# Kernel tuning notes

Measured on AMD Instinct MI355X. Metric: run time of the kernel, lower is better.

Reference implementation:

```python
import jax, jax.numpy as jnp
import numpy as np

B, L, K, I, O = 4, 10000, 16, 256, 256


def setup_inputs() -> dict:
    key = jax.random.key(0)
    k1, k2, k3 = jax.random.split(key, 3)
    x = jax.random.normal(k1, (B, L, I), dtype=jnp.float32)
    index_tensor = jax.random.randint(k2, (L, K), 0, L, dtype=jnp.int64)
    stdv = 0.5
    mask = jax.random.uniform(k3, (K, I, O), dtype=jnp.float32, minval=-stdv, maxval=stdv)
    bias = jnp.zeros((O,), dtype=jnp.float32)
    return {"x": x, "index_tensor": index_tensor, "mask": mask, "bias": bias}


def reference(x, index_tensor, mask, bias):
    # torch: expand x to [b,l,l,i], gather along dim2 with index[l,k] -> [b,l,k,i]
    # equivalent: per output node n, neighbors x[:, index_tensor[n, j], :]
    gathered = x[:, index_tensor, :]            # [b, l, k, i]
    # flatten(k,i) @ flatten(mask: [k*i, o]) == einsum over k,i
    y = jnp.einsum('blki,kio->blo', gathered, mask) + bias
    return y
```

## Files before the change

### kernel.cpp

```cpp
#include <hip/hip_runtime.h>

#define Bdim 4
#define Ldim 10000
#define Kdim 16
#define Idim 256
#define Odim 256

typedef __attribute__((ext_vector_type(8))) __bf16 bf16x8;
typedef __attribute__((ext_vector_type(4))) float f32x4;

__global__ __launch_bounds__(256)
void prepack(const float* __restrict__ x, const float* __restrict__ mask,
             __bf16* __restrict__ xb, __bf16* __restrict__ wpk)
{
    const int b = blockIdx.x;
    if (b < 2500) {
        const size_t base = ((size_t)b * 256 + threadIdx.x) * 16;
#pragma unroll
        for (int j = 0; j < 2; ++j) {
            const float4 f0 = *(const float4*)(x + base + j * 8);
            const float4 f1 = *(const float4*)(x + base + j * 8 + 4);
            bf16x8 v;
            v[0] = (__bf16)f0.x; v[1] = (__bf16)f0.y; v[2] = (__bf16)f0.z; v[3] = (__bf16)f0.w;
            v[4] = (__bf16)f1.x; v[5] = (__bf16)f1.y; v[6] = (__bf16)f1.z; v[7] = (__bf16)f1.w;
            *(bf16x8*)(xb + base + j * 8) = v;
        }
    } else {
        const int tg = (b - 2500) * 256 + threadIdx.x;
        const int c  = tg >> 6;
        const int ln = tg & 63;
        const int ni  = c & 3;
        const int ks  = (c >> 2) & 1;
        const int wid = (c >> 3) & 3;
        const int kb  = c >> 5;
        const int n   = wid * 64 + ni * 16 + (ln & 15);
        const int kk0 = kb * 64 + ks * 32 + (ln >> 4) * 8;
        bf16x8 v;
#pragma unroll
        for (int j = 0; j < 8; ++j)
            v[j] = (__bf16)mask[(size_t)(kk0 + j) * Odim + n];
        *(bf16x8*)(wpk + (size_t)tg * 8) = v;
    }
}

#define TL 16
#define BM 64
#define LDA 72

#define BARRIER() do { asm volatile("s_waitcnt lgkmcnt(0)" ::: "memory"); \
                       __builtin_amdgcn_s_barrier(); } while (0)

__global__ __launch_bounds__(256, 3)
void piconv_gemm(const __bf16* __restrict__ xb,
                 const int* __restrict__ idxT,
                 const __bf16* __restrict__ wpk,
                 const float* __restrict__ bias,
                 float* __restrict__ out)
{
    __shared__ __bf16 Alds[2][BM * LDA];
    __shared__ int    idx_lds[TL * Kdim];

    const int t    = threadIdx.x;
    const int l0   = blockIdx.x * TL;
    const int lane = t & 63;
    const int wid  = t >> 6;
    const int q    = lane >> 4;
    const int r16  = lane & 15;

    idx_lds[t] = idxT[l0 * Kdim + t];

    const int arow  = t >> 2;
    const int apart = t & 3;
    const int alt   = arow & 15;
    const int abb   = arow >> 4;
    const size_t abase = ((size_t)abb * Ldim) << 8;

    const __bf16* wbase = wpk + ((size_t)(wid * 8) << 9) + lane * 8;

    f32x4  acc[4][4] = {};
    bf16x8 a0lo, a0hi;
    bf16x8 a1lo, a1hi;
    bf16x8 wA[8], wB[8];

    __syncthreads();

    {
        const int iv = idx_lds[alt * Kdim];
        const __bf16* s0 = xb + abase + (((size_t)iv) << 8) + apart * 16;
        a0lo = *(const bf16x8*)s0;
        a0hi = *(const bf16x8*)(s0 + 8);
#pragma unroll
        for (int j = 0; j < 8; ++j)
            wA[j] = *(const bf16x8*)(wbase + j * 512);
        const __bf16* s1 = s0 + 64;
        a1lo = *(const bf16x8*)s1;
        a1hi = *(const bf16x8*)(s1 + 8);
    }

#define STEP(KB, BUF, ALO, AHI, WCUR, WNXT, PFA, PFW)                           \
    {                                                                           \
        *(bf16x8*)&Alds[BUF][arow * LDA + apart * 16]     = ALO;                \
        *(bf16x8*)&Alds[BUF][arow * LDA + apart * 16 + 8] = AHI;                \
        BARRIER();                                                              \
        if (PFA) {                       \
            const int kn = ((KB) + 2) >> 2;                                     \
            const int io = ((((KB) + 2) & 3) << 6) + apart * 16;                \
            const int iv = idx_lds[alt * Kdim + kn];                            \
            const __bf16* s = xb + abase + (((size_t)iv) << 8) + io;            \
            ALO = *(const bf16x8*)s;                                            \
            AHI = *(const bf16x8*)(s + 8);                                      \
        }                                                                       \
        if (PFW) {                                                 \
            const __bf16* wq = wbase + ((size_t)((KB) + 1)) * 16384;            \
            _Pragma("unroll")                                                   \
            for (int j = 0; j < 8; ++j)                                         \
                WNXT[j] = *(const bf16x8*)(wq + j * 512);                       \
        }                                                                       \
        _Pragma("unroll")                                                       \
        for (int ks = 0; ks < 2; ++ks) {                                        \
            bf16x8 af[4];                                                       \
            _Pragma("unroll")                                                   \
            for (int mi = 0; mi < 4; ++mi)                                      \
                af[mi] = *(bf16x8*)&Alds[BUF][(mi * 16 + r16) * LDA + ks * 32 + q * 8]; \
            _Pragma("unroll")                                                   \
            for (int mi = 0; mi < 4; ++mi)                                      \
                _Pragma("unroll")                                               \
                for (int ni = 0; ni < 4; ++ni)                                  \
                    acc[mi][ni] = __builtin_amdgcn_mfma_f32_16x16x32_bf16(      \
                        af[mi], WCUR[ks * 4 + ni], acc[mi][ni], 0, 0, 0);       \
        }                                                                       \
    }

    for (int kb2 = 0; kb2 < 31; ++kb2) {
        STEP(2 * kb2,     0, a0lo, a0hi, wA, wB, true, true)
        STEP(2 * kb2 + 1, 1, a1lo, a1hi, wB, wA, true, true)
    }
    STEP(62, 0, a0lo, a0hi, wA, wB, false, true)
    STEP(63, 1, a1lo, a1hi, wB, wA, false, false)
#undef STEP

    float bv[4];
#pragma unroll
    for (int ni = 0; ni < 4; ++ni)
        bv[ni] = bias[wid * 64 + ni * 16 + r16];
#pragma unroll
    for (int mi = 0; mi < 4; ++mi) {
#pragma unroll
        for (int rr = 0; rr < 4; ++rr) {
            const int lt = q * 4 + rr;
            float* dst = out + (((size_t)(mi * Ldim + l0 + lt)) << 8) + wid * 64 + r16;
#pragma unroll
            for (int ni = 0; ni < 4; ++ni)
                dst[ni * 16] = acc[mi][ni][rr] + bv[ni];
        }
    }
}

#define FTL 32
#define FBN 128
#define FLDA 72
__global__ __launch_bounds__(256)
void piconv_fallback(const float* __restrict__ x,
                     const int* __restrict__ idxT,
                     const float* __restrict__ mask,
                     const float* __restrict__ bias,
                     float* __restrict__ out)
{
    __shared__ __bf16 Alds[128 * FLDA];
    __shared__ __bf16 Wlds[FBN * FLDA];
    const int t  = threadIdx.x;
    const int l0 = blockIdx.x * FTL;
    const int n0 = blockIdx.y * FBN;
    const int lane = t & 63;
    const int wid  = t >> 6;
    const int wm   = wid >> 1;
    const int wn   = wid & 1;
    const int q    = lane >> 4;
    const int r16  = lane & 15;
    f32x4 acc[4][4] = {};
    const int am    = t >> 1;
    const int ahalf = t & 1;
    const int alt   = am & 31;
    const int abb   = am >> 5;
    const int al    = l0 + alt;
    const bool avalid = (al < Ldim);
    for (int kb = 0; kb < 64; ++kb) {
        {
            const int ksl = kb >> 2;
            const int i0  = ((kb & 3) << 6) + (ahalf << 5);
            const int idx = avalid ? idxT[al * Kdim + ksl] : 0;
            const float* src = x + (((size_t)(abb * Ldim + idx)) << 8) + i0;
#pragma unroll
            for (int j = 0; j < 4; ++j) {
                const float4 f0 = *(const float4*)(src + j * 8);
                const float4 f1 = *(const float4*)(src + j * 8 + 4);
                bf16x8 v;
                v[0] = (__bf16)f0.x; v[1] = (__bf16)f0.y; v[2] = (__bf16)f0.z; v[3] = (__bf16)f0.w;
                v[4] = (__bf16)f1.x; v[5] = (__bf16)f1.y; v[6] = (__bf16)f1.z; v[7] = (__bf16)f1.w;
                *(bf16x8*)&Alds[am * FLDA + (ahalf << 5) + j * 8] = v;
            }
        }
        {
#pragma unroll
            for (int it = 0; it < 4; ++it) {
                const int pair = t + it * 256;
                const int n    = pair & 127;
                const int g    = pair >> 7;
                const float* src = mask + (((size_t)(kb * 64 + g * 8)) << 8) + n0 + n;
                bf16x8 v;
#pragma unroll
                for (int j = 0; j < 8; ++j)
                    v[j] = (__bf16)src[(size_t)j << 8];
                *(bf16x8*)&Wlds[n * FLDA + g * 8] = v;
            }
        }
        __syncthreads();
#pragma unroll
        for (int ks = 0; ks < 2; ++ks) {
            bf16x8 af[4], bfr[4];
#pragma unroll
            for (int mi = 0; mi < 4; ++mi)
                af[mi] = *(bf16x8*)&Alds[(wm * 64 + mi * 16 + r16) * FLDA + ks * 32 + q * 8];
#pragma unroll
            for (int ni = 0; ni < 4; ++ni)
                bfr[ni] = *(bf16x8*)&Wlds[(wn * 64 + ni * 16 + r16) * FLDA + ks * 32 + q * 8];
#pragma unroll
            for (int mi = 0; mi < 4; ++mi)
#pragma unroll
                for (int ni = 0; ni < 4; ++ni)
                    acc[mi][ni] = __builtin_amdgcn_mfma_f32_16x16x32_bf16(
                        af[mi], bfr[ni], acc[mi][ni], 0, 0, 0);
        }
        __syncthreads();
    }
    float bv[4];
#pragma unroll
    for (int ni = 0; ni < 4; ++ni)
        bv[ni] = bias[n0 + wn * 64 + ni * 16 + r16];
#pragma unroll
    for (int mi = 0; mi < 4; ++mi) {
        const int mrow = wm * 64 + mi * 16 + q * 4;
#pragma unroll
        for (int rr = 0; rr < 4; ++rr) {
            const int m  = mrow + rr;
            const int lt = m & 31;
            const int bb = m >> 5;
            const int l  = l0 + lt;
            if (l < Ldim) {
                float* dst = out + (((size_t)(bb * Ldim + l)) << 8) + n0 + wn * 64 + r16;
#pragma unroll
                for (int ni = 0; ni < 4; ++ni)
                    dst[ni * 16] = acc[mi][ni][rr] + bv[ni];
            }
        }
    }
}

extern "C" void kernel_launch(void* const* d_in, const int* in_sizes, int n_in,
                              void* d_out, int out_size, void* d_ws, size_t ws_size,
                              hipStream_t stream) {
    const float* x    = (const float*)d_in[0];
    const int*   idx  = (const int*)d_in[1];
    const float* mask = (const float*)d_in[2];
    const float* bias = (const float*)d_in[3];
    float* out = (float*)d_out;

    const size_t xb_bytes = (size_t)Bdim * Ldim * Idim * 2;
    const size_t wp_bytes = (size_t)Kdim * Idim * Odim * 2;

    if (ws_size >= xb_bytes + wp_bytes) {
        __bf16* xb  = (__bf16*)d_ws;
        __bf16* wpk = (__bf16*)((char*)d_ws + xb_bytes);
        prepack<<<2500 + 512, 256, 0, stream>>>(x, mask, xb, wpk);
        piconv_gemm<<<Ldim / TL, 256, 0, stream>>>(xb, idx, wpk, bias, out);
    } else {
        dim3 grid((Ldim + FTL - 1) / FTL, Odim / FBN, 1);
        piconv_fallback<<<grid, 256, 0, stream>>>(x, idx, mask, bias, out);
    }
}
```

Before: 184.9 us.

## Split GEMM output columns across two 128-thread blocks per L-tile

Each L-tile is now handled by two blocks of two waves, each covering half of the output columns, instead of one block of four waves covering all 256 columns. Every thread gathers twice as much A data per step, and the gathered A tile is loaded redundantly by both blocks. The aim is more, smaller blocks for better occupancy and scheduling across CUs, at the cost of duplicated gather traffic and LDS writes.

```diff
diff --git a/kernel.cpp b/kernel.cpp
--- a/kernel.cpp
+++ b/kernel.cpp
@@ -50,7 +50,7 @@
 #define BARRIER() do { asm volatile("s_waitcnt lgkmcnt(0)" ::: "memory"); \
                        __builtin_amdgcn_s_barrier(); } while (0)
 
-__global__ __launch_bounds__(256, 3)
+__global__ __launch_bounds__(128, 2)
 void piconv_gemm(const __bf16* __restrict__ xb,
                  const int* __restrict__ idxT,
                  const __bf16* __restrict__ wpk,
@@ -63,55 +63,67 @@
     const int t    = threadIdx.x;
     const int l0   = blockIdx.x * TL;
     const int lane = t & 63;
-    const int wid  = t >> 6;
+    const int gq   = blockIdx.y * 2 + (t >> 6);
     const int q    = lane >> 4;
     const int r16  = lane & 15;
 
-    idx_lds[t] = idxT[l0 * Kdim + t];
-
-    const int arow  = t >> 2;
-    const int apart = t & 3;
-    const int alt   = arow & 15;
-    const int abb   = arow >> 4;
+    idx_lds[t]       = idxT[l0 * Kdim + t];
+    idx_lds[t + 128] = idxT[l0 * Kdim + t + 128];
+
+    const int arow = t >> 1;
+    const int ah   = t & 1;
+    const int alt  = arow & 15;
+    const int abb  = arow >> 4;
     const size_t abase = ((size_t)abb * Ldim) << 8;
 
-    const __bf16* wbase = wpk + ((size_t)(wid * 8) << 9) + lane * 8;
+    const __bf16* wbase = wpk + ((size_t)(gq * 8) << 9) + lane * 8;
 
     f32x4  acc[4][4] = {};
-    bf16x8 a0lo, a0hi;
-    bf16x8 a1lo, a1hi;
+    bf16x8 a0v0, a0v1, a0v2, a0v3;
+    bf16x8 a1v0, a1v1, a1v2, a1v3;
     bf16x8 wA[8], wB[8];
 
     __syncthreads();
 
     {
         const int iv = idx_lds[alt * Kdim];
-        const __bf16* s0 = xb + abase + (((size_t)iv) << 8) + apart * 16;
-        a0lo = *(const bf16x8*)s0;
-        a0hi = *(const bf16x8*)(s0 + 8);
+        const __bf16* s0 = xb + abase + (((size_t)iv) << 8) + ah * 32;
+        a0v0 = *(const bf16x8*)(s0);
+        a0v1 = *(const bf16x8*)(s0 + 8);
+        a0v2 = *(const bf16x8*)(s0 + 16);
+        a0v3 = *(const bf16x8*)(s0 + 24);
 #pragma unroll
         for (int j = 0; j < 8; ++j)
             wA[j] = *(const bf16x8*)(wbase + j * 512);
         const __bf16* s1 = s0 + 64;
-        a1lo = *(const bf16x8*)s1;
-        a1hi = *(const bf16x8*)(s1 + 8);
-    }
-
-#define STEP(KB, BUF, ALO, AHI, WCUR, WNXT, PFA, PFW)                           \
+        a1v0 = *(const bf16x8*)(s1);
+        a1v1 = *(const bf16x8*)(s1 + 8);
+        a1v2 = *(const bf16x8*)(s1 + 16);
+        a1v3 = *(const bf16x8*)(s1 + 24);
+    }
+
+#define STEP(S, BUF, AV0, AV1, AV2, AV3, WCUR, WNXT, PFA, PFW)                  \
     {                                                                           \
-        *(bf16x8*)&Alds[BUF][arow * LDA + apart * 16]     = ALO;                \
-        *(bf16x8*)&Alds[BUF][arow * LDA + apart * 16 + 8] = AHI;                \
+        {                                                                       \
+            __bf16* d = &Alds[BUF][arow * LDA + ah * 32];                       \
+            *(bf16x8*)(d)      = AV0;                                           \
+            *(bf16x8*)(d + 8)  = AV1;                                           \
+            *(bf16x8*)(d + 16) = AV2;                                           \
+            *(bf16x8*)(d + 24) = AV3;                                           \
+        }                                                                       \
         BARRIER();                                                              \
-        if (PFA) {                       \
-            const int kn = ((KB) + 2) >> 2;                                     \
-            const int io = ((((KB) + 2) & 3) << 6) + apart * 16;                \
+        if (PFA) {                        \
+            const int kn = ((S) + 2) >> 2;                                      \
+            const int io = ((((S) + 2) & 3) << 6) + ah * 32;                    \
             const int iv = idx_lds[alt * Kdim + kn];                            \
             const __bf16* s = xb + abase + (((size_t)iv) << 8) + io;            \
-            ALO = *(const bf16x8*)s;                                            \
-            AHI = *(const bf16x8*)(s + 8);                                      \
-        }                                                                       \
-        if (PFW) {                                                 \
-            const __bf16* wq = wbase + ((size_t)((KB) + 1)) * 16384;            \
+            AV0 = *(const bf16x8*)(s);                                          \
+            AV1 = *(const bf16x8*)(s + 8);                                      \
+            AV2 = *(const bf16x8*)(s + 16);                                     \
+            AV3 = *(const bf16x8*)(s + 24);                                     \
+        }                                                                       \
+        if (PFW) {                                                  \
+            const __bf16* wq = wbase + ((size_t)((S) + 1)) * 16384;             \
             _Pragma("unroll")                                                   \
             for (int j = 0; j < 8; ++j)                                         \
                 WNXT[j] = *(const bf16x8*)(wq + j * 512);                       \
@@ -131,24 +143,24 @@
         }                                                                       \
     }
 
-    for (int kb2 = 0; kb2 < 31; ++kb2) {
-        STEP(2 * kb2,     0, a0lo, a0hi, wA, wB, true, true)
-        STEP(2 * kb2 + 1, 1, a1lo, a1hi, wB, wA, true, true)
-    }
-    STEP(62, 0, a0lo, a0hi, wA, wB, false, true)
-    STEP(63, 1, a1lo, a1hi, wB, wA, false, false)
+    for (int s2 = 0; s2 < 31; ++s2) {
+        STEP(2 * s2,     0, a0v0, a0v1, a0v2, a0v3, wA, wB, true, true)
+        STEP(2 * s2 + 1, 1, a1v0, a1v1, a1v2, a1v3, wB, wA, true, true)
+    }
+    STEP(62, 0, a0v0, a0v1, a0v2, a0v3, wA, wB, false, true)
+    STEP(63, 1, a1v0, a1v1, a1v2, a1v3, wB, wA, false, false)
 #undef STEP
 
     float bv[4];
 #pragma unroll
     for (int ni = 0; ni < 4; ++ni)
-        bv[ni] = bias[wid * 64 + ni * 16 + r16];
+        bv[ni] = bias[gq * 64 + ni * 16 + r16];
 #pragma unroll
     for (int mi = 0; mi < 4; ++mi) {
 #pragma unroll
         for (int rr = 0; rr < 4; ++rr) {
             const int lt = q * 4 + rr;
-            float* dst = out + (((size_t)(mi * Ldim + l0 + lt)) << 8) + wid * 64 + r16;
+            float* dst = out + (((size_t)(mi * Ldim + l0 + lt)) << 8) + gq * 64 + r16;
 #pragma unroll
             for (int ni = 0; ni < 4; ++ni)
                 dst[ni * 16] = acc[mi][ni][rr] + bv[ni];
@@ -272,7 +284,8 @@
         __bf16* xb  = (__bf16*)d_ws;
         __bf16* wpk = (__bf16*)((char*)d_ws + xb_bytes);
         prepack<<<2500 + 512, 256, 0, stream>>>(x, mask, xb, wpk);
-        piconv_gemm<<<Ldim / TL, 256, 0, stream>>>(xb, idx, wpk, bias, out);
+        dim3 ggrid(Ldim / TL, 2, 1);
+        piconv_gemm<<<ggrid, 128, 0, stream>>>(xb, idx, wpk, bias, out);
     } else {
         dim3 grid((Ldim + FTL - 1) / FTL, Odim / FBN, 1);
         piconv_fallback<<<grid, 256, 0, stream>>>(x, idx, mask, bias, out);
```

Result: slower. 216.0 us (+16.8%).
